# Optimization experiments

Measured on AMD Instinct MI355X. Metric: run time of the kernel, lower is better.

## Reference

```python
import jax, jax.numpy as jnp
import numpy as np

VOCAB, DIM, SEQ, DEPTH, WS, MULT = 32, 256, 8192, 6, 512, 4
BATCH = 2
NEG = -1e9  # mask fill value


def setup_inputs():
    key = jax.random.key(0)
    ks = jax.random.split(key, 8)
    L, d, h = DEPTH, DIM, DIM * MULT
    s = 0.02
    return {
        "tokens": jax.random.randint(ks[0], (BATCH, SEQ), 0, VOCAB),
        "embed": jax.random.normal(ks[1], (VOCAB, d)) * s,
        "ff_ln_s": jnp.ones((L, d)),
        "ff_ln_b": jnp.zeros((L, d)),
        "w1": jax.random.normal(ks[2], (L, d, h)) * s,
        "b1": jnp.zeros((L, h)),
        "w2": jax.random.normal(ks[3], (L, h, d)) * s,
        "b2": jnp.zeros((L, d)),
        "lnf_s": jnp.ones((d,)),
        "lnf_b": jnp.zeros((d,)),
        "w_out": jax.random.normal(ks[4], (d, VOCAB)) * s,
        "b_out": jnp.zeros((VOCAB,)),
    }


def layer_norm(x, s, b, eps=1e-5):
    m = jnp.mean(x, axis=-1, keepdims=True)
    v = jnp.var(x, axis=-1, keepdims=True)
    return (x - m) * jax.lax.rsqrt(v + eps) * s + b


def rotate_half(x):
    x1, x2 = jnp.split(x, 2, axis=-1)
    return jnp.concatenate([-x2, x1], axis=-1)


def local_attn(x, ws):
    # lucidrains LocalAttention: causal, look_backward=1, look_forward=0,
    # exact_windowsize=True, rotary pos emb on q/k. q = k = v = x (no projections).
    b, n, d = x.shape
    inv_freq = 1.0 / (10000.0 ** (jnp.arange(0, d, 2, dtype=jnp.float32) / d))
    t = jnp.arange(n, dtype=jnp.float32)
    fr = t[:, None] * inv_freq[None, :]
    fr = jnp.concatenate([fr, fr], axis=-1)  # (n, d)
    qk = x * jnp.cos(fr) + rotate_half(x) * jnp.sin(fr)  # rotary applied to q and k (identical)
    w = n // ws
    bq = qk.reshape(b, w, ws, d)
    bk = bq  # q == k here
    bv = x.reshape(b, w, ws, d)
    # look_around: each window sees [previous window, current window]
    pk = jnp.pad(bk, ((0, 0), (1, 0), (0, 0), (0, 0)))[:, :-1]
    pv = jnp.pad(bv, ((0, 0), (1, 0), (0, 0), (0, 0)))[:, :-1]
    bk2 = jnp.concatenate([pk, bk], axis=2)  # (b, w, 2*ws, d)
    bv2 = jnp.concatenate([pv, bv], axis=2)
    tq = jnp.arange(n).reshape(w, ws)
    tp = jnp.pad(tq, ((1, 0), (0, 0)), constant_values=-1)[:-1]
    tk = jnp.concatenate([tp, tq], axis=1)  # (w, 2*ws), -1 marks pad
    allowed = (
        (tk[:, None, :] >= 0)
        & (tq[:, :, None] >= tk[:, None, :])          # causal
        & (tq[:, :, None] <= tk[:, None, :] + ws)     # exact windowsize (look_backward=1)
    )
    sim = jnp.einsum("bwid,bwjd->bwij", bq, bk2) * (d ** -0.5)
    sim = jnp.where(allowed[None], sim, NEG)
    attn = jax.nn.softmax(sim, axis=-1)
    out = jnp.einsum("bwij,bwjd->bwid", attn, bv2)
    return out.reshape(b, n, d)


def reference(tokens, embed, ff_ln_s, ff_ln_b, w1, b1, w2, b2, lnf_s, lnf_b, w_out, b_out):
    x = embed[tokens]  # (b, n, d)
    for i in range(DEPTH):
        x = x + local_attn(x, WS)
        h = layer_norm(x, ff_ln_s[i], ff_ln_b[i])
        h = jax.nn.gelu(h @ w1[i] + b1[i], approximate=False)
        x = x + (h @ w2[i] + b2[i])
    return layer_norm(x, lnf_s, lnf_b) @ w_out + b_out  # (b, n, vocab)
```

## Files before the change

kernel.cpp:

```cpp
#include <hip/hip_runtime.h>
#include <hip/hip_bf16.h>
#include <math.h>

#define BATCH 2
#define SEQL 8192
#define DD 256
#define HDIM 1024
#define NLAYER 6
#define WSZ 512
#define NVOCAB 32
#define NTOK (BATCH*SEQL)
#define PLN (DD*HDIM)

typedef unsigned short u16;
typedef __attribute__((ext_vector_type(8))) short bf16x8;
typedef __attribute__((ext_vector_type(4))) float f32x4;

union B8 { uint4 u; bf16x8 b; ushort s[8]; uint w[4]; };

__device__ inline float bf2f(u16 v){
  unsigned int u = ((unsigned int)v) << 16;
  return __uint_as_float(u);
}
__device__ inline u16 f2bf(float f){
  unsigned int u = __float_as_uint(f);
  u += 0x7fff + ((u >> 16) & 1);
  return (u16)(u >> 16);
}

__device__ __forceinline__ void gload16(const void* g, void* l){
  __builtin_amdgcn_global_load_lds(
      (const __attribute__((address_space(1))) unsigned int*)g,
      (__attribute__((address_space(3))) unsigned int*)l, 16, 0, 0);
}

__global__ void k_tables(float* __restrict__ ct, float* __restrict__ st){
  int idx = blockIdx.x * 256 + threadIdx.x;
  if (idx >= SEQL * 128) return;
  int t = idx >> 7, i = idx & 127;
  float freq = expf(-((float)i / 128.0f) * 9.210340371976184f);
  float fr = (float)t * freq;
  ct[idx] = cosf(fr);
  st[idx] = sinf(fr);
}

__global__ void k_embed(const int* __restrict__ tokens, const float* __restrict__ emb,
                        float* __restrict__ x){
  int vbid = (blockIdx.x & 7) * 512 + (blockIdx.x >> 3);
  int idx = vbid * 256 + threadIdx.x;
  int bt = idx >> 6, dv = (idx & 63) << 2;
  int tok = tokens[bt];
  *(float4*)(x + bt * DD + dv) = *(const float4*)(emb + tok * DD + dv);
}

__global__ void k_rope(const float* __restrict__ x, const float* __restrict__ ct,
                       const float* __restrict__ st, u16* __restrict__ qk,
                       u16* __restrict__ xv){
  int vbid = (blockIdx.x & 7) * 256 + (blockIdx.x >> 3);
  int idx = vbid * 256 + threadIdx.x;
  int bt = idx >> 5, iv = (idx & 31) << 2;
  int t = bt & (SEQL - 1);
  const float* xr = x + bt * DD;
  float4 x1 = *(const float4*)(xr + iv);
  float4 x2 = *(const float4*)(xr + 128 + iv);
  float4 c = *(const float4*)(ct + t * 128 + iv);
  float4 s = *(const float4*)(st + t * 128 + iv);
  ushort4 q1, q2, v1, v2;
  q1.x = f2bf(x1.x * c.x - x2.x * s.x);  q2.x = f2bf(x2.x * c.x + x1.x * s.x);
  q1.y = f2bf(x1.y * c.y - x2.y * s.y);  q2.y = f2bf(x2.y * c.y + x1.y * s.y);
  q1.z = f2bf(x1.z * c.z - x2.z * s.z);  q2.z = f2bf(x2.z * c.z + x1.z * s.z);
  q1.w = f2bf(x1.w * c.w - x2.w * s.w);  q2.w = f2bf(x2.w * c.w + x1.w * s.w);
  v1.x = f2bf(x1.x); v1.y = f2bf(x1.y); v1.z = f2bf(x1.z); v1.w = f2bf(x1.w);
  v2.x = f2bf(x2.x); v2.y = f2bf(x2.y); v2.z = f2bf(x2.z); v2.w = f2bf(x2.w);
  *(ushort4*)(qk + bt * DD + iv)       = q1;
  *(ushort4*)(qk + bt * DD + 128 + iv) = q2;
  *(ushort4*)(xv + bt * DD + iv)       = v1;
  *(ushort4*)(xv + bt * DD + 128 + iv) = v2;
}

__global__ void __launch_bounds__(512, 2) k_attn2(const u16* __restrict__ qk,
                                                  const u16* __restrict__ xv,
                                                  const float* __restrict__ x,
                                                  float* __restrict__ y,
                                                  const float* __restrict__ g,
                                                  const float* __restrict__ b,
                                                  u16* __restrict__ lnx,
                                                  int fuse){
  __shared__ char smem[131072];

  const int tid = threadIdx.x;
  const int lane = tid & 63;
  const int w = tid >> 6;
  const int qh = w >> 1, kh = w & 1;
  const int l15 = lane & 15, lg = lane >> 4;

  const int qg = (blockIdx.x & 7) * 32 + (blockIdx.x >> 3);
  const int qb = qg * 64;
  const int t0 = qb & (SEQL - 1);
  const size_t bbase = (size_t)(qb >> 13) << 13;

  uint4 qf[8];
  {
    const u16* qr = qk + (size_t)(qb + qh*16 + l15) * DD + lg*4;
    #pragma unroll
    for (int s = 0; s < 8; ++s){
      uint2 a = *(const uint2*)(qr + s*32);
      uint2 bq = *(const uint2*)(qr + s*32 + 16);
      qf[s] = make_uint4(a.x, a.y, bq.x, bq.y);
    }
  }

  f32x4 oacc[16];
  #pragma unroll
  for (int d = 0; d < 16; ++d) oacc[d] = (f32x4){0.f, 0.f, 0.f, 0.f};
  float lacc = 0.f;

  const int p0 = (t0 >= WSZ) ? (t0 - WSZ) : 0;
  const int ntile = ((t0 - p0) >> 6) + 1;

  const int sk15 = tid & 15, skt = (tid >> 4) & 3, sc = tid >> 6;
  const int sdh = tid & 31, sk0 = (tid >> 5) * 4;
  const int vkhw = sk0 >> 5, vh = (sk0 >> 4) & 1, vlgw = (sk0 >> 2) & 3;

  uint4 kreg[4];
  uint  vreg[4][4];

  {
    const u16* sb = qk + (bbase + (size_t)p0 + skt*16 + sk15) * DD;
    #pragma unroll
    for (int u = 0; u < 4; ++u) kreg[u] = *(const uint4*)(sb + u*64 + sc*8);
    #pragma unroll
    for (int u = 0; u < 4; ++u){
      int d0 = sdh*2 + u*64;
      const u16* vb = xv + (bbase + (size_t)p0 + sk0) * DD + d0;
      vreg[u][0] = *(const uint*)(vb);
      vreg[u][1] = *(const uint*)(vb + DD);
      vreg[u][2] = *(const uint*)(vb + 2*DD);
      vreg[u][3] = *(const uint*)(vb + 3*DD);
    }
  }
  #pragma unroll
  for (int u = 0; u < 4; ++u){
    int d0 = u*64 + sc*8;
    int s = d0 >> 5, r = d0 & 31;
    int h = r >> 4, lgw = (r & 15) >> 2;
    int rec = ((s*4 + skt)*4 + lgw)*16 + sk15;
    char* wp = smem + rec*16 + h*8;
    *(uint2*)wp         = make_uint2(kreg[u].x, kreg[u].y);
    *(uint2*)(wp + 256) = make_uint2(kreg[u].z, kreg[u].w);
  }
  #pragma unroll
  for (int u = 0; u < 4; ++u){
    int d0 = sdh*2 + u*64;
    uint a0 = vreg[u][0], a1 = vreg[u][1], a2 = vreg[u][2], a3 = vreg[u][3];
    uint w0 = (a0 & 0xffffu) | (a1 << 16);
    uint w1 = (a2 & 0xffffu) | (a3 << 16);
    uint w2 = (a0 >> 16) | (a1 & 0xffff0000u);
    uint w3 = (a2 >> 16) | (a3 & 0xffff0000u);
    int dimt = d0 >> 4, d15 = d0 & 15;
    int rec = ((dimt*2 + vkhw)*4 + vlgw)*16 + d15;
    char* wp = smem + 32768 + rec*16 + vh*8;
    *(uint2*)wp        = make_uint2(w0, w1);
    *(uint2*)(wp + 16) = make_uint2(w2, w3);
  }
  __syncthreads();

  int cur = 0;
  for (int ti = 0; ti < ntile; ++ti){
    const int p = p0 + ti*64;
    if (ti + 1 < ntile){
      const int pn = p + 64;
      const u16* sb = qk + (bbase + (size_t)pn + skt*16 + sk15) * DD;
      #pragma unroll
      for (int u = 0; u < 4; ++u) kreg[u] = *(const uint4*)(sb + u*64 + sc*8);
      #pragma unroll
      for (int u = 0; u < 4; ++u){
        int d0 = sdh*2 + u*64;
        const u16* vb = xv + (bbase + (size_t)pn + sk0) * DD + d0;
        vreg[u][0] = *(const uint*)(vb);
        vreg[u][1] = *(const uint*)(vb + DD);
        vreg[u][2] = *(const uint*)(vb + 2*DD);
        vreg[u][3] = *(const uint*)(vb + 3*DD);
      }
    }

    char* Klds = smem + cur*65536;
    char* Vlds = Klds + 32768;

    f32x4 sacc[2];
    sacc[0] = (f32x4){0.f,0.f,0.f,0.f};
    sacc[1] = (f32x4){0.f,0.f,0.f,0.f};
    #pragma unroll
    for (int s = 0; s < 8; ++s){
      B8 ka0, ka1, qbf;
      ka0.b = *(const bf16x8*)(Klds + (((s*4 + kh*2+0)*4 + lg)*16 + l15)*16);
      ka1.b = *(const bf16x8*)(Klds + (((s*4 + kh*2+1)*4 + lg)*16 + l15)*16);
      qbf.u = qf[s];
      sacc[0] = __builtin_amdgcn_mfma_f32_16x16x32_bf16(ka0.b, qbf.b, sacc[0], 0, 0, 0);
      sacc[1] = __builtin_amdgcn_mfma_f32_16x16x32_bf16(ka1.b, qbf.b, sacc[1], 0, 0, 0);
    }

    B8 pa;
    #pragma unroll
    for (int ktp = 0; ktp < 2; ++ktp){
      int kbase = p + kh*32 + ktp*16 + lg*4;
      int qpos = t0 + qh*16 + l15;
      #pragma unroll
      for (int r = 0; r < 4; ++r){
        int kpos = kbase + r;
        float sv = sacc[ktp][r] * 0.0625f;
        bool ok = (kpos <= qpos) && (qpos <= kpos + WSZ);
        float pv = ok ? __expf(sv) : 0.0f;
        lacc += pv;
        pa.s[ktp*4 + r] = f2bf(pv);
      }
    }

    #pragma unroll
    for (int dimt = 0; dimt < 16; ++dimt){
      B8 vb;
      vb.b = *(const bf16x8*)(Vlds + (((dimt*2 + kh)*4 + lg)*16 + l15)*16);
      oacc[dimt] = __builtin_amdgcn_mfma_f32_16x16x32_bf16(pa.b, vb.b, oacc[dimt], 0, 0, 0);
    }

    if (ti + 1 < ntile){
      char* nK = smem + (cur ^ 1)*65536;
      char* nV = nK + 32768;
      #pragma unroll
      for (int u = 0; u < 4; ++u){
        int d0 = u*64 + sc*8;
        int s = d0 >> 5, r = d0 & 31;
        int h = r >> 4, lgw = (r & 15) >> 2;
        int rec = ((s*4 + skt)*4 + lgw)*16 + sk15;
        char* wp = nK + rec*16 + h*8;
        *(uint2*)wp         = make_uint2(kreg[u].x, kreg[u].y);
        *(uint2*)(wp + 256) = make_uint2(kreg[u].z, kreg[u].w);
      }
      #pragma unroll
      for (int u = 0; u < 4; ++u){
        int d0 = sdh*2 + u*64;
        uint a0 = vreg[u][0], a1 = vreg[u][1], a2 = vreg[u][2], a3 = vreg[u][3];
        uint w0 = (a0 & 0xffffu) | (a1 << 16);
        uint w1 = (a2 & 0xffffu) | (a3 << 16);
        uint w2 = (a0 >> 16) | (a1 & 0xffff0000u);
        uint w3 = (a2 >> 16) | (a3 & 0xffff0000u);
        int dimt = d0 >> 4, d15 = d0 & 15;
        int rec = ((dimt*2 + vkhw)*4 + vlgw)*16 + d15;
        char* wp = nV + rec*16 + vh*8;
        *(uint2*)wp        = make_uint2(w0, w1);
        *(uint2*)(wp + 16) = make_uint2(w2, w3);
      }
    }
    __syncthreads();
    cur ^= 1;
  }

  float* Obuf = (float*)smem;
  float* redl = (float*)(smem + 67584);

  const int q = tid >> 3, dv = (tid & 7) * 4;
  float4 xrs[8];
  #pragma unroll
  for (int pass = 0; pass < 8; ++pass)
    xrs[pass] = *(const float4*)(x + (size_t)(qb + q)*DD + pass*32 + dv);

  lacc += __shfl_xor(lacc, 16, 64);
  lacc += __shfl_xor(lacc, 32, 64);
  if (lane < 16) redl[kh*64 + qh*16 + l15] = lacc;
  if (kh == 0){
    #pragma unroll
    for (int dimt = 0; dimt < 16; ++dimt)
      #pragma unroll
      for (int r = 0; r < 4; ++r)
        Obuf[(qh*16 + lg*4 + r)*264 + dimt*16 + l15] = oacc[dimt][r];
  }
  __syncthreads();
  if (kh == 1){
    #pragma unroll
    for (int dimt = 0; dimt < 16; ++dimt)
      #pragma unroll
      for (int r = 0; r < 4; ++r)
        Obuf[(qh*16 + lg*4 + r)*264 + dimt*16 + l15] += oacc[dimt][r];
  }
  __syncthreads();

  float inv = 1.0f / (redl[q] + redl[64 + q]);
  float4 ovs[8];
  float lsum = 0.f, lss = 0.f;
  #pragma unroll
  for (int pass = 0; pass < 8; ++pass){
    float4 o = *(float4*)&Obuf[q*264 + pass*32 + dv];
    float4 ov;
    ov.x = xrs[pass].x + o.x * inv;
    ov.y = xrs[pass].y + o.y * inv;
    ov.z = xrs[pass].z + o.z * inv;
    ov.w = xrs[pass].w + o.w * inv;
    *(float4*)(y + (size_t)(qb + q)*DD + pass*32 + dv) = ov;
    ovs[pass] = ov;
    lsum += ov.x + ov.y + ov.z + ov.w;
    lss  += ov.x*ov.x + ov.y*ov.y + ov.z*ov.z + ov.w*ov.w;
  }

  if (fuse){
    #pragma unroll
    for (int o = 1; o < 8; o <<= 1){
      lsum += __shfl_xor(lsum, o, 64);
      lss  += __shfl_xor(lss,  o, 64);
    }
    float m = lsum * (1.0f / DD);
    float var = lss * (1.0f / DD) - m * m;
    float rs = rsqrtf(var + 1e-5f);
    #pragma unroll
    for (int pass = 0; pass < 8; ++pass){
      float4 gf = *(const float4*)(g + pass*32 + dv);
      float4 bf = *(const float4*)(b + pass*32 + dv);
      ushort4 o4;
      o4.x = f2bf((ovs[pass].x - m) * rs * gf.x + bf.x);
      o4.y = f2bf((ovs[pass].y - m) * rs * gf.y + bf.y);
      o4.z = f2bf((ovs[pass].z - m) * rs * gf.z + bf.z);
      o4.w = f2bf((ovs[pass].w - m) * rs * gf.w + bf.w);
      *(ushort4*)(lnx + (size_t)(qb + q) * DD + pass*32 + dv) = o4;
    }
  }
}

__global__ void __launch_bounds__(256) k_ln(const float* __restrict__ in,
                                            const float* __restrict__ g,
                                            const float* __restrict__ b,
                                            u16* __restrict__ out){
  int wid = (blockIdx.x * 256 + threadIdx.x) >> 6;
  int lane = threadIdx.x & 63;
  float4 v = *(const float4*)(in + wid * DD + lane * 4);
  float s = v.x + v.y + v.z + v.w;
  float ss = v.x * v.x + v.y * v.y + v.z * v.z + v.w * v.w;
  #pragma unroll
  for (int o = 32; o; o >>= 1){ s += __shfl_xor(s, o, 64); ss += __shfl_xor(ss, o, 64); }
  float m = s * (1.0f / DD);
  float var = ss * (1.0f / DD) - m * m;
  float rs = rsqrtf(var + 1e-5f);
  float4 gf = *(const float4*)(g + lane * 4);
  float4 bf = *(const float4*)(b + lane * 4);
  ushort4 o4;
  o4.x = f2bf((v.x - m) * rs * gf.x + bf.x);
  o4.y = f2bf((v.y - m) * rs * gf.y + bf.y);
  o4.z = f2bf((v.z - m) * rs * gf.z + bf.z);
  o4.w = f2bf((v.w - m) * rs * gf.w + bf.w);
  *(ushort4*)(out + wid * DD + lane * 4) = o4;
}

template<int KDIM, int NDIM>
__device__ __forceinline__ void split_one(const float* __restrict__ W,
                                          u16* __restrict__ Phi, int idx){
  int c15 = idx & 15;
  int lg = (idx >> 4) & 3;
  int nt = (idx >> 6) % (NDIM/16);
  int ks = idx / ((NDIM/16) * 64);
  int col = nt*16 + c15;
  B8 hi;
  #pragma unroll
  for (int j = 0; j < 8; ++j){
    int k = ks*32 + (j >> 2)*16 + lg*4 + (j & 3);
    hi.s[j] = f2bf(W[(size_t)k * NDIM + col]);
  }
  *(uint4*)(Phi + (size_t)idx * 8) = hi.u;
}

__global__ void __launch_bounds__(256) k_splitall(const float* __restrict__ w1,
                                                  const float* __restrict__ w2,
                                                  u16* __restrict__ P){
  int bk = blockIdx.x;
  int L = bk >> 8, r = bk & 255;
  u16* PL = P + (size_t)L * 2 * PLN;
  if (r < 128) split_one<DD, HDIM>(w1 + (size_t)L*PLN, PL, r*256 + threadIdx.x);
  else         split_one<HDIM, DD>(w2 + (size_t)L*PLN, PL + PLN, (r-128)*256 + threadIdx.x);
}

template<int KDIM, int NDIM, int EPI>
__global__ void __launch_bounds__(256, 4) k_gemm(const u16* __restrict__ A,
                                              const u16* __restrict__ BhG,
                                              const float* __restrict__ bias,
                                              const float* __restrict__ res,
                                              float* __restrict__ outf,
                                              u16* __restrict__ outh){
  __shared__ char smem[18432 + 8192];
  char* As = smem;
  char* Bs = smem + 18432;

  const int tid = threadIdx.x;
  const int lane = tid & 63;
  const int w = tid >> 6;
  const int wr = w >> 1, wc = w & 1;
  const int l15 = lane & 15, lg = lane >> 4;
  const int lin = blockIdx.x;
  const int xcd = lin & 7;
  const int idx = lin >> 3;
  const int m0 = (xcd * 16 + (idx & 15)) * 128;
  const int n0 = (idx >> 4) * 64;
  const int NT16 = NDIM / 16;

  f32x4 acc[4][2];
  #pragma unroll
  for (int a = 0; a < 4; ++a){
    acc[a][0] = (f32x4){0.f,0.f,0.f,0.f};
    acc[a][1] = (f32x4){0.f,0.f,0.f,0.f};
  }

  for (int kb = 0; kb < KDIM/64; ++kb){
    __syncthreads();
    #pragma unroll
    for (int p = 0; p < 4; ++p){
      int c = p*256 + tid;
      int row = c >> 3, cc = c & 7;
      uint4 v = *(const uint4*)(A + (size_t)(m0 + row) * KDIM + kb*64 + cc*8);
      *(uint4*)(As + row*144 + cc*16) = v;
    }
    #pragma unroll
    for (int p = 0; p < 2; ++p){
      int j = p*256 + tid;
      int chunk = j >> 6, r = j & 63;
      const u16* src = BhG
          + (((size_t)(kb*2 + (chunk >> 2)) * NT16 + (n0 >> 4) + (chunk & 3))*64 + r)*8;
      gload16(src, Bs + j*16);
    }
    __syncthreads();

    #pragma unroll
    for (int s = 0; s < 2; ++s){
      B8 af[4], bhf[2];
      #pragma unroll
      for (int a = 0; a < 4; ++a){
        const char* ab = As + (wr*64 + a*16 + l15)*144 + s*64 + lg*8;
        uint2 lo = *(const uint2*)ab;
        uint2 hi = *(const uint2*)(ab + 32);
        af[a].u = make_uint4(lo.x, lo.y, hi.x, hi.y);
      }
      #pragma unroll
      for (int c = 0; c < 2; ++c){
        int off = (((s*4 + wc*2 + c)*64) + lg*16 + l15)*16;
        bhf[c].u = *(const uint4*)(Bs + off);
      }
      #pragma unroll
      for (int a = 0; a < 4; ++a)
        #pragma unroll
        for (int c = 0; c < 2; ++c)
          acc[a][c] = __builtin_amdgcn_mfma_f32_16x16x32_bf16(af[a].b, bhf[c].b, acc[a][c], 0, 0, 0);
    }
  }

  float bv[2];
  bv[0] = bias[n0 + wc*32 + l15];
  bv[1] = bias[n0 + wc*32 + 16 + l15];

  #pragma unroll
  for (int a = 0; a < 4; ++a){
    #pragma unroll
    for (int c = 0; c < 2; ++c){
      #pragma unroll
      for (int r = 0; r < 4; ++r){
        int row = m0 + wr*64 + a*16 + lg*4 + r;
        int col = n0 + wc*32 + c*16 + l15;
        float v = acc[a][c][r] + bv[c];
        if (EPI == 0){
          float gl = 0.5f * v * (1.0f + erff(v * 0.70710678f));
          outh[(size_t)row * NDIM + col] = f2bf(gl);
        } else {
          outf[(size_t)row * NDIM + col] = v + res[(size_t)row * NDIM + col];
        }
      }
    }
  }
}

__global__ void __launch_bounds__(256) k_final(const float* __restrict__ x,
                                               const float* __restrict__ g,
                                               const float* __restrict__ b,
                                               const float* __restrict__ wout,
                                               const float* __restrict__ bout,
                                               float* __restrict__ out){
  __shared__ float lds[4][256];
  int vbid = (blockIdx.x & 7) * 512 + (blockIdx.x >> 3);
  int widx = threadIdx.x >> 6, lane = threadIdx.x & 63;
  int bt = vbid * 4 + widx;
  float4 v = *(const float4*)(x + bt * DD + lane * 4);
  float s = v.x + v.y + v.z + v.w;
  float ss = v.x * v.x + v.y * v.y + v.z * v.z + v.w * v.w;
  #pragma unroll
  for (int o = 32; o; o >>= 1){ s += __shfl_xor(s, o, 64); ss += __shfl_xor(ss, o, 64); }
  float m = s * (1.0f / DD);
  float var = ss * (1.0f / DD) - m * m;
  float rs = rsqrtf(var + 1e-5f);
  float4 gf = *(const float4*)(g + lane * 4);
  float4 bf = *(const float4*)(b + lane * 4);
  lds[widx][lane * 4 + 0] = (v.x - m) * rs * gf.x + bf.x;
  lds[widx][lane * 4 + 1] = (v.y - m) * rs * gf.y + bf.y;
  lds[widx][lane * 4 + 2] = (v.z - m) * rs * gf.z + bf.z;
  lds[widx][lane * 4 + 3] = (v.w - m) * rs * gf.w + bf.w;
  __syncthreads();
  int vo = lane & 31, half = lane >> 5;
  const float* lp = &lds[widx][half * 128];
  const float* wp = wout + half * 128 * NVOCAB + vo;
  float acc = 0;
  #pragma unroll 4
  for (int d = 0; d < 128; ++d) acc += lp[d] * wp[d * NVOCAB];
  acc += __shfl_down(acc, 32, 64);
  if (lane < 32) out[bt * NVOCAB + vo] = acc + bout[vo];
}

extern "C" void kernel_launch(void* const* d_in, const int* in_sizes, int n_in,
                              void* d_out, int out_size, void* d_ws, size_t ws_size,
                              hipStream_t stream) {
  const int*   tokens = (const int*)d_in[0];
  const float* emb   = (const float*)d_in[1];
  const float* ffs   = (const float*)d_in[2];
  const float* ffb   = (const float*)d_in[3];
  const float* w1    = (const float*)d_in[4];
  const float* b1    = (const float*)d_in[5];
  const float* w2    = (const float*)d_in[6];
  const float* b2    = (const float*)d_in[7];
  const float* lnfs  = (const float*)d_in[8];
  const float* lnfb  = (const float*)d_in[9];
  const float* wout  = (const float*)d_in[10];
  const float* bout  = (const float*)d_in[11];
  float* out = (float*)d_out;

  char* ws = (char*)d_ws;
  float* x    = (float*)(ws);
  float* y    = (float*)(ws + (size_t)16*1024*1024);
  u16*   buf8 = (u16*)  (ws + (size_t)32*1024*1024);
  u16*   qk   = (u16*)  (ws + (size_t)40*1024*1024);
  u16*   pln  = (u16*)  (ws + (size_t)48*1024*1024);
  u16*   h    = (u16*)  (ws + (size_t)56*1024*1024);

  float* ct = (float*)(ws + (size_t)96*1024*1024);
  float* st = (float*)(ws + (size_t)100*1024*1024);
  const int bigws = (ws_size >= (size_t)104*1024*1024) ? 1 : 0;
  if (!bigws){
    ct = (float*)(ws + (size_t)48*1024*1024);
    st = (float*)(ws + (size_t)52*1024*1024);
  }
  const int fuse = (ws_size >= (size_t)96*1024*1024) ? 1 : 0;
  u16* lnx = fuse ? (u16*)(ws + (size_t)88*1024*1024) : buf8;

  k_tables<<<4096, 256, 0, stream>>>(ct, st);
  k_embed<<<4096, 256, 0, stream>>>(tokens, emb, x);
  if (bigws) k_splitall<<<1536, 256, 0, stream>>>(w1, w2, pln);
  for (int L = 0; L < NLAYER; ++L){
    k_rope<<<2048, 256, 0, stream>>>(x, ct, st, qk, buf8);
    k_attn2<<<256, 512, 0, stream>>>(qk, buf8, x, y,
                                     ffs + L*DD, ffb + L*DD, lnx, fuse);
    if (!fuse)
      k_ln<<<4096, 256, 0, stream>>>(y, ffs + L*DD, ffb + L*DD, lnx);
    const u16* PL;
    if (bigws){
      PL = pln + (size_t)L*2*PLN;
    } else {
      k_splitall<<<256, 256, 0, stream>>>(w1 + (size_t)L*PLN, w2 + (size_t)L*PLN, qk);
      PL = qk;
    }
    k_gemm<DD, HDIM, 0><<<2048, 256, 0, stream>>>(
        lnx, PL, b1 + L*HDIM, nullptr, nullptr, h);
    k_gemm<HDIM, DD, 1><<<512, 256, 0, stream>>>(
        h, PL + PLN, b2 + L*DD, y, x, nullptr);
  }
  k_final<<<4096, 256, 0, stream>>>(x, lnfs, lnfb, wout, bout, out);
}
```

Measured before the change: 676.7 us.

## Store V transposed from rope kernel and read V fragments directly from global

```diff
diff --git a/kernel.cpp b/kernel.cpp
--- a/kernel.cpp
+++ b/kernel.cpp
@@ -53,40 +53,54 @@
   *(float4*)(x + bt * DD + dv) = *(const float4*)(emb + tok * DD + dv);
 }
 
-__global__ void k_rope(const float* __restrict__ x, const float* __restrict__ ct,
-                       const float* __restrict__ st, u16* __restrict__ qk,
-                       u16* __restrict__ xv){
-  int vbid = (blockIdx.x & 7) * 256 + (blockIdx.x >> 3);
-  int idx = vbid * 256 + threadIdx.x;
-  int bt = idx >> 5, iv = (idx & 31) << 2;
-  int t = bt & (SEQL - 1);
-  const float* xr = x + bt * DD;
-  float4 x1 = *(const float4*)(xr + iv);
-  float4 x2 = *(const float4*)(xr + 128 + iv);
-  float4 c = *(const float4*)(ct + t * 128 + iv);
-  float4 s = *(const float4*)(st + t * 128 + iv);
-  ushort4 q1, q2, v1, v2;
-  q1.x = f2bf(x1.x * c.x - x2.x * s.x);  q2.x = f2bf(x2.x * c.x + x1.x * s.x);
-  q1.y = f2bf(x1.y * c.y - x2.y * s.y);  q2.y = f2bf(x2.y * c.y + x1.y * s.y);
-  q1.z = f2bf(x1.z * c.z - x2.z * s.z);  q2.z = f2bf(x2.z * c.z + x1.z * s.z);
-  q1.w = f2bf(x1.w * c.w - x2.w * s.w);  q2.w = f2bf(x2.w * c.w + x1.w * s.w);
-  v1.x = f2bf(x1.x); v1.y = f2bf(x1.y); v1.z = f2bf(x1.z); v1.w = f2bf(x1.w);
-  v2.x = f2bf(x2.x); v2.y = f2bf(x2.y); v2.z = f2bf(x2.z); v2.w = f2bf(x2.w);
-  *(ushort4*)(qk + bt * DD + iv)       = q1;
-  *(ushort4*)(qk + bt * DD + 128 + iv) = q2;
-  *(ushort4*)(xv + bt * DD + iv)       = v1;
-  *(ushort4*)(xv + bt * DD + 128 + iv) = v2;
+__global__ void __launch_bounds__(256) k_rope2(const float* __restrict__ x,
+                                               const float* __restrict__ ct,
+                                               const float* __restrict__ st,
+                                               u16* __restrict__ qk,
+                                               u16* __restrict__ xvT){
+  __shared__ u16 vt[256][66];
+  const int tid = threadIdx.x;
+  const int vbid = (blockIdx.x & 7) * 32 + (blockIdx.x >> 3);
+  const int tok0 = vbid * 64;
+
+  #pragma unroll
+  for (int u = 0; u < 32; ++u){
+    int e = u*256 + tid;
+    int tok = e >> 7, i = e & 127;
+    int row = tok0 + tok;
+    int t = row & (SEQL - 1);
+    float x1 = x[(size_t)row*DD + i];
+    float x2 = x[(size_t)row*DD + 128 + i];
+    float c = ct[t*128 + i], s = st[t*128 + i];
+    qk[(size_t)row*DD + i]       = f2bf(x1*c - x2*s);
+    qk[(size_t)row*DD + 128 + i] = f2bf(x2*c + x1*s);
+    vt[i][tok]       = f2bf(x1);
+    vt[i + 128][tok] = f2bf(x2);
+  }
+  __syncthreads();
+
+  const int batch = tok0 >> 13;
+  const int tloc = tok0 & (SEQL - 1);
+  #pragma unroll
+  for (int u = 0; u < 8; ++u){
+    int j = u*256 + tid;
+    int dim = j >> 3, tg = j & 7;
+    B8 pk;
+    #pragma unroll
+    for (int e = 0; e < 8; ++e) pk.s[e] = vt[dim][tg*8 + e];
+    *(uint4*)(xvT + ((size_t)batch*DD + dim)*SEQL + tloc + tg*8) = pk.u;
+  }
 }
 
 __global__ void __launch_bounds__(512, 2) k_attn2(const u16* __restrict__ qk,
-                                                  const u16* __restrict__ xv,
+                                                  const u16* __restrict__ xvT,
                                                   const float* __restrict__ x,
                                                   float* __restrict__ y,
                                                   const float* __restrict__ g,
                                                   const float* __restrict__ b,
                                                   u16* __restrict__ lnx,
                                                   int fuse){
-  __shared__ char smem[131072];
+  __shared__ char smem[68096];
 
   const int tid = threadIdx.x;
   const int lane = tid & 63;
@@ -97,7 +111,8 @@
   const int qg = (blockIdx.x & 7) * 32 + (blockIdx.x >> 3);
   const int qb = qg * 64;
   const int t0 = qb & (SEQL - 1);
-  const size_t bbase = (size_t)(qb >> 13) << 13;
+  const int batch = qb >> 13;
+  const size_t bbase = (size_t)batch << 13;
 
   uint4 qf[8];
   {
@@ -119,25 +134,13 @@
   const int ntile = ((t0 - p0) >> 6) + 1;
 
   const int sk15 = tid & 15, skt = (tid >> 4) & 3, sc = tid >> 6;
-  const int sdh = tid & 31, sk0 = (tid >> 5) * 4;
-  const int vkhw = sk0 >> 5, vh = (sk0 >> 4) & 1, vlgw = (sk0 >> 2) & 3;
 
   uint4 kreg[4];
-  uint  vreg[4][4];
 
   {
     const u16* sb = qk + (bbase + (size_t)p0 + skt*16 + sk15) * DD;
     #pragma unroll
     for (int u = 0; u < 4; ++u) kreg[u] = *(const uint4*)(sb + u*64 + sc*8);
-    #pragma unroll
-    for (int u = 0; u < 4; ++u){
-      int d0 = sdh*2 + u*64;
-      const u16* vb = xv + (bbase + (size_t)p0 + sk0) * DD + d0;
-      vreg[u][0] = *(const uint*)(vb);
-      vreg[u][1] = *(const uint*)(vb + DD);
-      vreg[u][2] = *(const uint*)(vb + 2*DD);
-      vreg[u][3] = *(const uint*)(vb + 3*DD);
-    }
   }
   #pragma unroll
   for (int u = 0; u < 4; ++u){
@@ -149,43 +152,18 @@
     *(uint2*)wp         = make_uint2(kreg[u].x, kreg[u].y);
     *(uint2*)(wp + 256) = make_uint2(kreg[u].z, kreg[u].w);
   }
-  #pragma unroll
-  for (int u = 0; u < 4; ++u){
-    int d0 = sdh*2 + u*64;
-    uint a0 = vreg[u][0], a1 = vreg[u][1], a2 = vreg[u][2], a3 = vreg[u][3];
-    uint w0 = (a0 & 0xffffu) | (a1 << 16);
-    uint w1 = (a2 & 0xffffu) | (a3 << 16);
-    uint w2 = (a0 >> 16) | (a1 & 0xffff0000u);
-    uint w3 = (a2 >> 16) | (a3 & 0xffff0000u);
-    int dimt = d0 >> 4, d15 = d0 & 15;
-    int rec = ((dimt*2 + vkhw)*4 + vlgw)*16 + d15;
-    char* wp = smem + 32768 + rec*16 + vh*8;
-    *(uint2*)wp        = make_uint2(w0, w1);
-    *(uint2*)(wp + 16) = make_uint2(w2, w3);
-  }
   __syncthreads();
 
   int cur = 0;
   for (int ti = 0; ti < ntile; ++ti){
     const int p = p0 + ti*64;
     if (ti + 1 < ntile){
-      const int pn = p + 64;
-      const u16* sb = qk + (bbase + (size_t)pn + skt*16 + sk15) * DD;
+      const u16* sb = qk + (bbase + (size_t)(p + 64) + skt*16 + sk15) * DD;
       #pragma unroll
       for (int u = 0; u < 4; ++u) kreg[u] = *(const uint4*)(sb + u*64 + sc*8);
-      #pragma unroll
-      for (int u = 0; u < 4; ++u){
-        int d0 = sdh*2 + u*64;
-        const u16* vb = xv + (bbase + (size_t)pn + sk0) * DD + d0;
-        vreg[u][0] = *(const uint*)(vb);
-        vreg[u][1] = *(const uint*)(vb + DD);
-        vreg[u][2] = *(const uint*)(vb + 2*DD);
-        vreg[u][3] = *(const uint*)(vb + 3*DD);
-      }
-    }
-
-    char* Klds = smem + cur*65536;
-    char* Vlds = Klds + 32768;
+    }
+
+    char* Klds = smem + cur*32768;
 
     f32x4 sacc[2];
     sacc[0] = (f32x4){0.f,0.f,0.f,0.f};
@@ -218,14 +196,16 @@
 
     #pragma unroll
     for (int dimt = 0; dimt < 16; ++dimt){
-      B8 vb;
-      vb.b = *(const bf16x8*)(Vlds + (((dimt*2 + kh)*4 + lg)*16 + l15)*16);
+      const u16* vr = xvT + ((size_t)(batch*DD + dimt*16 + l15))*SEQL
+                          + p + kh*32 + lg*4;
+      uint2 a = *(const uint2*)vr;
+      uint2 bq = *(const uint2*)(vr + 16);
+      B8 vb; vb.u = make_uint4(a.x, a.y, bq.x, bq.y);
       oacc[dimt] = __builtin_amdgcn_mfma_f32_16x16x32_bf16(pa.b, vb.b, oacc[dimt], 0, 0, 0);
     }
 
     if (ti + 1 < ntile){
-      char* nK = smem + (cur ^ 1)*65536;
-      char* nV = nK + 32768;
+      char* nK = smem + (cur ^ 1)*32768;
       #pragma unroll
       for (int u = 0; u < 4; ++u){
         int d0 = u*64 + sc*8;
@@ -235,20 +215,6 @@
         char* wp = nK + rec*16 + h*8;
         *(uint2*)wp         = make_uint2(kreg[u].x, kreg[u].y);
         *(uint2*)(wp + 256) = make_uint2(kreg[u].z, kreg[u].w);
-      }
-      #pragma unroll
-      for (int u = 0; u < 4; ++u){
-        int d0 = sdh*2 + u*64;
-        uint a0 = vreg[u][0], a1 = vreg[u][1], a2 = vreg[u][2], a3 = vreg[u][3];
-        uint w0 = (a0 & 0xffffu) | (a1 << 16);
-        uint w1 = (a2 & 0xffffu) | (a3 << 16);
-        uint w2 = (a0 >> 16) | (a1 & 0xffff0000u);
-        uint w3 = (a2 >> 16) | (a3 & 0xffff0000u);
-        int dimt = d0 >> 4, d15 = d0 & 15;
-        int rec = ((dimt*2 + vkhw)*4 + vlgw)*16 + d15;
-        char* wp = nV + rec*16 + vh*8;
-        *(uint2*)wp        = make_uint2(w0, w1);
-        *(uint2*)(wp + 16) = make_uint2(w2, w3);
       }
     }
     __syncthreads();
@@ -545,7 +511,7 @@
   k_embed<<<4096, 256, 0, stream>>>(tokens, emb, x);
   if (bigws) k_splitall<<<1536, 256, 0, stream>>>(w1, w2, pln);
   for (int L = 0; L < NLAYER; ++L){
-    k_rope<<<2048, 256, 0, stream>>>(x, ct, st, qk, buf8);
+    k_rope2<<<256, 256, 0, stream>>>(x, ct, st, qk, buf8);
     k_attn2<<<256, 512, 0, stream>>>(qk, buf8, x, y,
                                      ffs + L*DD, ffb + L*DD, lnx, fuse);
     if (!fuse)
```

Result: slower. 945.0 us (+39.7%).

## Store rope tables and attention residual in bf16, merge init kernels

Applied to the files above, without the earlier changes.

```diff
diff --git a/kernel.cpp b/kernel.cpp
--- a/kernel.cpp
+++ b/kernel.cpp
@@ -34,28 +34,27 @@
       (__attribute__((address_space(3))) unsigned int*)l, 16, 0, 0);
 }
 
-__global__ void k_tables(float* __restrict__ ct, float* __restrict__ st){
-  int idx = blockIdx.x * 256 + threadIdx.x;
-  if (idx >= SEQL * 128) return;
-  int t = idx >> 7, i = idx & 127;
-  float freq = expf(-((float)i / 128.0f) * 9.210340371976184f);
-  float fr = (float)t * freq;
-  ct[idx] = cosf(fr);
-  st[idx] = sinf(fr);
-}
-
-__global__ void k_embed(const int* __restrict__ tokens, const float* __restrict__ emb,
-                        float* __restrict__ x){
-  int vbid = (blockIdx.x & 7) * 512 + (blockIdx.x >> 3);
-  int idx = vbid * 256 + threadIdx.x;
-  int bt = idx >> 6, dv = (idx & 63) << 2;
-  int tok = tokens[bt];
-  *(float4*)(x + bt * DD + dv) = *(const float4*)(emb + tok * DD + dv);
-}
-
-__global__ void k_rope(const float* __restrict__ x, const float* __restrict__ ct,
-                       const float* __restrict__ st, u16* __restrict__ qk,
-                       u16* __restrict__ xv){
+__global__ void k_init(const int* __restrict__ tokens, const float* __restrict__ emb,
+                       float* __restrict__ x, uint* __restrict__ cs){
+  if (blockIdx.x < 4096){
+    int idx = blockIdx.x * 256 + threadIdx.x;
+    int t = idx >> 7, i = idx & 127;
+    float freq = expf(-((float)i / 128.0f) * 9.210340371976184f);
+    float fr = (float)t * freq;
+    uint c = (uint)f2bf(cosf(fr));
+    uint s = (uint)f2bf(sinf(fr));
+    cs[idx] = c | (s << 16);
+  } else {
+    int vbid = blockIdx.x - 4096;
+    int idx = vbid * 256 + threadIdx.x;
+    int bt = idx >> 6, dv = (idx & 63) << 2;
+    int tok = tokens[bt];
+    *(float4*)(x + bt * DD + dv) = *(const float4*)(emb + tok * DD + dv);
+  }
+}
+
+__global__ void k_rope(const float* __restrict__ x, const uint* __restrict__ cs,
+                       u16* __restrict__ qk, u16* __restrict__ xv){
   int vbid = (blockIdx.x & 7) * 256 + (blockIdx.x >> 3);
   int idx = vbid * 256 + threadIdx.x;
   int bt = idx >> 5, iv = (idx & 31) << 2;
@@ -63,13 +62,16 @@
   const float* xr = x + bt * DD;
   float4 x1 = *(const float4*)(xr + iv);
   float4 x2 = *(const float4*)(xr + 128 + iv);
-  float4 c = *(const float4*)(ct + t * 128 + iv);
-  float4 s = *(const float4*)(st + t * 128 + iv);
+  uint4 p = *(const uint4*)(cs + t * 128 + iv);
+  float c0 = bf2f((u16)(p.x & 0xffff)), s0 = bf2f((u16)(p.x >> 16));
+  float c1 = bf2f((u16)(p.y & 0xffff)), s1 = bf2f((u16)(p.y >> 16));
+  float c2 = bf2f((u16)(p.z & 0xffff)), s2 = bf2f((u16)(p.z >> 16));
+  float c3 = bf2f((u16)(p.w & 0xffff)), s3 = bf2f((u16)(p.w >> 16));
   ushort4 q1, q2, v1, v2;
-  q1.x = f2bf(x1.x * c.x - x2.x * s.x);  q2.x = f2bf(x2.x * c.x + x1.x * s.x);
-  q1.y = f2bf(x1.y * c.y - x2.y * s.y);  q2.y = f2bf(x2.y * c.y + x1.y * s.y);
-  q1.z = f2bf(x1.z * c.z - x2.z * s.z);  q2.z = f2bf(x2.z * c.z + x1.z * s.z);
-  q1.w = f2bf(x1.w * c.w - x2.w * s.w);  q2.w = f2bf(x2.w * c.w + x1.w * s.w);
+  q1.x = f2bf(x1.x * c0 - x2.x * s0);  q2.x = f2bf(x2.x * c0 + x1.x * s0);
+  q1.y = f2bf(x1.y * c1 - x2.y * s1);  q2.y = f2bf(x2.y * c1 + x1.y * s1);
+  q1.z = f2bf(x1.z * c2 - x2.z * s2);  q2.z = f2bf(x2.z * c2 + x1.z * s2);
+  q1.w = f2bf(x1.w * c3 - x2.w * s3);  q2.w = f2bf(x2.w * c3 + x1.w * s3);
   v1.x = f2bf(x1.x); v1.y = f2bf(x1.y); v1.z = f2bf(x1.z); v1.w = f2bf(x1.w);
   v2.x = f2bf(x2.x); v2.y = f2bf(x2.y); v2.z = f2bf(x2.z); v2.w = f2bf(x2.w);
   *(ushort4*)(qk + bt * DD + iv)       = q1;
@@ -81,7 +83,7 @@
 __global__ void __launch_bounds__(512, 2) k_attn2(const u16* __restrict__ qk,
                                                   const u16* __restrict__ xv,
                                                   const float* __restrict__ x,
-                                                  float* __restrict__ y,
+                                                  u16* __restrict__ yb,
                                                   const float* __restrict__ g,
                                                   const float* __restrict__ b,
                                                   u16* __restrict__ lnx,
@@ -295,7 +297,9 @@
     ov.y = xrs[pass].y + o.y * inv;
     ov.z = xrs[pass].z + o.z * inv;
     ov.w = xrs[pass].w + o.w * inv;
-    *(float4*)(y + (size_t)(qb + q)*DD + pass*32 + dv) = ov;
+    ushort4 yv;
+    yv.x = f2bf(ov.x); yv.y = f2bf(ov.y); yv.z = f2bf(ov.z); yv.w = f2bf(ov.w);
+    *(ushort4*)(yb + (size_t)(qb + q)*DD + pass*32 + dv) = yv;
     ovs[pass] = ov;
     lsum += ov.x + ov.y + ov.z + ov.w;
     lss  += ov.x*ov.x + ov.y*ov.y + ov.z*ov.z + ov.w*ov.w;
@@ -324,13 +328,14 @@
   }
 }
 
-__global__ void __launch_bounds__(256) k_ln(const float* __restrict__ in,
+__global__ void __launch_bounds__(256) k_ln(const u16* __restrict__ in,
                                             const float* __restrict__ g,
                                             const float* __restrict__ b,
                                             u16* __restrict__ out){
   int wid = (blockIdx.x * 256 + threadIdx.x) >> 6;
   int lane = threadIdx.x & 63;
-  float4 v = *(const float4*)(in + wid * DD + lane * 4);
+  ushort4 i4 = *(const ushort4*)(in + (size_t)wid * DD + lane * 4);
+  float4 v = make_float4(bf2f(i4.x), bf2f(i4.y), bf2f(i4.z), bf2f(i4.w));
   float s = v.x + v.y + v.z + v.w;
   float ss = v.x * v.x + v.y * v.y + v.z * v.z + v.w * v.w;
   #pragma unroll
@@ -345,7 +350,7 @@
   o4.y = f2bf((v.y - m) * rs * gf.y + bf.y);
   o4.z = f2bf((v.z - m) * rs * gf.z + bf.z);
   o4.w = f2bf((v.w - m) * rs * gf.w + bf.w);
-  *(ushort4*)(out + wid * DD + lane * 4) = o4;
+  *(ushort4*)(out + (size_t)wid * DD + lane * 4) = o4;
 }
 
 template<int KDIM, int NDIM>
@@ -379,7 +384,7 @@
 __global__ void __launch_bounds__(256, 4) k_gemm(const u16* __restrict__ A,
                                               const u16* __restrict__ BhG,
                                               const float* __restrict__ bias,
-                                              const float* __restrict__ res,
+                                              const u16* __restrict__ res,
                                               float* __restrict__ outf,
                                               u16* __restrict__ outh){
   __shared__ char smem[18432 + 8192];
@@ -464,7 +469,7 @@
           float gl = 0.5f * v * (1.0f + erff(v * 0.70710678f));
           outh[(size_t)row * NDIM + col] = f2bf(gl);
         } else {
-          outf[(size_t)row * NDIM + col] = v + res[(size_t)row * NDIM + col];
+          outf[(size_t)row * NDIM + col] = v + bf2f(res[(size_t)row * NDIM + col]);
         }
       }
     }
@@ -525,27 +530,24 @@
 
   char* ws = (char*)d_ws;
   float* x    = (float*)(ws);
-  float* y    = (float*)(ws + (size_t)16*1024*1024);
+  u16*   y    = (u16*)  (ws + (size_t)16*1024*1024);
   u16*   buf8 = (u16*)  (ws + (size_t)32*1024*1024);
   u16*   qk   = (u16*)  (ws + (size_t)40*1024*1024);
   u16*   pln  = (u16*)  (ws + (size_t)48*1024*1024);
   u16*   h    = (u16*)  (ws + (size_t)56*1024*1024);
 
-  float* ct = (float*)(ws + (size_t)96*1024*1024);
-  float* st = (float*)(ws + (size_t)100*1024*1024);
+  uint* cs = (uint*)(ws + (size_t)96*1024*1024);
   const int bigws = (ws_size >= (size_t)104*1024*1024) ? 1 : 0;
   if (!bigws){
-    ct = (float*)(ws + (size_t)48*1024*1024);
-    st = (float*)(ws + (size_t)52*1024*1024);
+    cs = (uint*)(ws + (size_t)48*1024*1024);
   }
   const int fuse = (ws_size >= (size_t)96*1024*1024) ? 1 : 0;
   u16* lnx = fuse ? (u16*)(ws + (size_t)88*1024*1024) : buf8;
 
-  k_tables<<<4096, 256, 0, stream>>>(ct, st);
-  k_embed<<<4096, 256, 0, stream>>>(tokens, emb, x);
+  k_init<<<8192, 256, 0, stream>>>(tokens, emb, x, cs);
   if (bigws) k_splitall<<<1536, 256, 0, stream>>>(w1, w2, pln);
   for (int L = 0; L < NLAYER; ++L){
-    k_rope<<<2048, 256, 0, stream>>>(x, ct, st, qk, buf8);
+    k_rope<<<2048, 256, 0, stream>>>(x, cs, qk, buf8);
     k_attn2<<<256, 512, 0, stream>>>(qk, buf8, x, y,
                                      ffs + L*DD, ffb + L*DD, lnx, fuse);
     if (!fuse)
```

After: 664.7 us. About the same (-1.8%).
